# Performance work log

Measured on AMD Instinct MI355X. Metric: run time of the kernel, lower is better.

## Reference

```python
import jax, jax.numpy as jnp
import numpy as np

LOG_2PI = float(np.log(2.0 * np.pi))


def setup_inputs() -> dict:
    key = jax.random.key(0)
    k1, k2, k3 = jax.random.split(key, 3)
    B, T, F, K = 16, 1024, 1024, 500
    X = jax.random.normal(k1, (B, T, F), dtype=jnp.float32)
    mu = jax.random.normal(k2, (K, F), dtype=jnp.float32)
    # cov must be positive for log(cov); uniform in [0.5, 1.5)
    cov = jax.random.uniform(k3, (K, F), dtype=jnp.float32) + 0.5
    return {"X": X, "mu": mu, "cov": cov}


def reference(X, mu, cov):
    # Diagonal-covariance GMM log-likelihoods: out[b,t,k] = log N(X[b,t]; mu[k], diag(cov[k]))
    # Algebraic expansion of 0.5*sum((x-mu)^2/cov) into two GEMMs + bias, avoiding
    # the BxTxKxF broadcast intermediate. Same math as the torch module.
    D = mu.shape[-1]
    inv_cov = 1.0 / cov                                   # (K, F)
    C = -0.5 * D * LOG_2PI - 0.5 * jnp.sum(jnp.log(cov), axis=-1)  # (K,)
    quad = jnp.einsum('btf,kf->btk', X * X, inv_cov)      # sum x^2/cov
    cross = jnp.einsum('btf,kf->btk', X, mu * inv_cov)    # sum x*mu/cov
    const = jnp.sum(mu * mu * inv_cov, axis=-1)           # (K,) sum mu^2/cov
    ULL = 0.5 * (quad - 2.0 * cross + const[None, None, :])
    return C[None, None, :] - ULL                         # (B, T, K)
```

## Files before the change

kernel.cpp:

```cpp
#include <hip/hip_runtime.h>
#include <hip/hip_bf16.h>


typedef __attribute__((ext_vector_type(8))) __bf16 bf16x8;
typedef __attribute__((ext_vector_type(4))) float  f32x4;

#define LOG_2PI 1.837877066409345339082f

constexpr int M_TOT = 16384;
constexpr int F_DIM = 1024;
constexpr int K_GMM = 500;
constexpr int N_PAD = 512;

constexpr int BM  = 128;
constexpr int BN  = 128;
constexpr int BKF = 32;
constexpr int NIT = F_DIM / BKF;

__device__ __forceinline__ void gload_lds16(const void* g, void* l) {
    __builtin_amdgcn_global_load_lds(
        (const __attribute__((address_space(1))) unsigned*)g,
        (__attribute__((address_space(3))) unsigned*)l, 16, 0, 0);
}

__device__ __forceinline__ unsigned pack_sq_x(float x) {
    __hip_bfloat162 h = __float22bfloat162_rn(make_float2(x * x, x));
    union { __hip_bfloat162 h; unsigned u; } cv;
    cv.h = h;
    return cv.u;
}

__global__ __launch_bounds__(256) void prep_w_kernel(
    const float* __restrict__ mu, const float* __restrict__ cov,
    unsigned* __restrict__ Wimg, float* __restrict__ bias)
{
    const int k = blockIdx.x;
    const int t = threadIdx.x;
    const int r  = k & 127;
    const int tt = k >> 7;
    const int rsw = r & 7;
    float sl = 0.f, sq = 0.f;
    #pragma unroll
    for (int j = 0; j < 4; ++j) {
        const int f  = t + j * 256;
        const int it = f >> 5;
        const int cc = (f >> 2) & 7;
        const int q  = f & 3;
        const int dw = (tt * 32 + it) * 4096 + r * 32 + ((cc ^ rsw) << 2) + q;
        if (k < K_GMM) {
            const float c = cov[k * F_DIM + f];
            const float m = mu[k * F_DIM + f];
            const float ic = 1.0f / c;
            __hip_bfloat162 h = __float22bfloat162_rn(make_float2(-0.5f * ic, m * ic));
            union { __hip_bfloat162 h; unsigned u; } cv; cv.h = h;
            Wimg[dw] = cv.u;
            sl += logf(c);
            sq += m * m * ic;
        } else {
            Wimg[dw] = 0u;
        }
    }
    #pragma unroll
    for (int off = 32; off > 0; off >>= 1) {
        sl += __shfl_down(sl, off, 64);
        sq += __shfl_down(sq, off, 64);
    }
    __shared__ float red[8];
    if ((t & 63) == 0) { red[(t >> 6) * 2] = sl; red[(t >> 6) * 2 + 1] = sq; }
    __syncthreads();
    if (t == 0) {
        const float SL = red[0] + red[2] + red[4] + red[6];
        const float SQ = red[1] + red[3] + red[5] + red[7];
        bias[k] = (k < K_GMM)
                ? (-0.5f * (F_DIM * LOG_2PI) - 0.5f * SL - 0.5f * SQ) : 0.f;
    }
}

__global__ __launch_bounds__(256, 2) void gemm_kernel(
    const float* __restrict__ X, const unsigned* __restrict__ Wimg,
    const float* __restrict__ bias, float* __restrict__ out)
{
    __shared__ __align__(16) char smem[81920];
    float* ep = reinterpret_cast<float*>(smem);

    const int bid    = blockIdx.x;
    const int m_base = (bid & 127) * BM;
    const int n_tile = bid >> 7;
    const int n_base = n_tile * BN;

    const int tid  = threadIdx.x;
    const int lane = tid & 63;
    const int wv   = tid >> 6;
    const int wr   = (wv >> 1) * 64;
    const int wc   = (wv & 1) * 64;
    const int hi   = lane >> 4;
    const int lo   = lane & 15;
    const int lsw  = lo & 7;

    const int sr = tid >> 1;
    const int sh = tid & 1;

    const float4* Xv   = reinterpret_cast<const float4*>(X);
    const char*   Wimc = reinterpret_cast<const char*>(Wimg);

    f32x4 acc[4][4];
    #pragma unroll
    for (int a = 0; a < 4; ++a)
        #pragma unroll
        for (int b = 0; b < 4; ++b)
            acc[a][b] = (f32x4){0.f, 0.f, 0.f, 0.f};

    auto stageB = [&](int itS, int bufS) {
        const char* gs = Wimc + (size_t)(n_tile * 32 + itS) * 16384;
        #pragma unroll
        for (int i = 0; i < 4; ++i)
            gload_lds16(gs + i * 4096 + wv * 1024 + lane * 16,
                        smem + 32768 + bufS * 16384 + i * 4096 + wv * 1024);
    };
    auto loadA = [&](int itS, float4* ar) {
        #pragma unroll
        for (int j = 0; j < 4; ++j)
            ar[j] = Xv[(m_base + sr) * (F_DIM / 4) + itS * 8 + sh * 4 + j];
    };
    auto packA = [&](const float4* ar, int ab) {
        unsigned short* Ad = reinterpret_cast<unsigned short*>(smem + ab * 16384);
        #pragma unroll
        for (int j = 0; j < 4; ++j) {
            const int chunk = (sh * 4 + j) ^ (sr & 7);
            uint4 wa;
            wa.x = pack_sq_x(ar[j].x);
            wa.y = pack_sq_x(ar[j].y);
            wa.z = pack_sq_x(ar[j].z);
            wa.w = pack_sq_x(ar[j].w);
            *reinterpret_cast<uint4*>(&Ad[sr * 64 + chunk * 8]) = wa;
        }
    };
    auto compute = [&](int ab, int bb) {
        const unsigned short* Asc =
            reinterpret_cast<const unsigned short*>(smem + ab * 16384);
        const unsigned short* Bsc =
            reinterpret_cast<const unsigned short*>(smem + 32768 + bb * 16384);
        #pragma unroll
        for (int c = 0; c < 2; ++c) {
            bf16x8 af[4], bf[4];
            #pragma unroll
            for (int a = 0; a < 4; ++a) {
                const int row   = wr + a * 16 + lo;
                const int chunk = (c * 4 + hi) ^ lsw;
                af[a] = *reinterpret_cast<const bf16x8*>(&Asc[row * 64 + chunk * 8]);
            }
            #pragma unroll
            for (int b = 0; b < 4; ++b) {
                const int row   = wc + b * 16 + lo;
                const int chunk = (c * 4 + hi) ^ lsw;
                bf[b] = *reinterpret_cast<const bf16x8*>(&Bsc[row * 64 + chunk * 8]);
            }
            #pragma unroll
            for (int a = 0; a < 4; ++a)
                #pragma unroll
                for (int b = 0; b < 4; ++b)
                    acc[a][b] = __builtin_amdgcn_mfma_f32_16x16x32_bf16(
                        af[a], bf[b], acc[a][b], 0, 0, 0);
        }
    };

    float4 aA[4], aB[4];
    stageB(0, 0);
    loadA(0, aB);
    stageB(1, 1);
    loadA(1, aA);
    packA(aB, 0);
    asm volatile("s_waitcnt vmcnt(8) lgkmcnt(0)" ::: "memory");
    __builtin_amdgcn_s_barrier();
    __builtin_amdgcn_sched_barrier(0);

    for (int it = 0; it < NIT; it += 2) {
        const int b0 = it % 3;
        const int b1 = (it + 1) % 3;
        const int b2 = (it + 2) % 3;
        const int b3 = (it + 3) % 3;

        if (it + 2 < NIT) { stageB(it + 2, b2); loadA(it + 2, aB); }
        compute(0, b0);
        packA(aA, 1);
        if (it + 2 < NIT)
            asm volatile("s_waitcnt vmcnt(8) lgkmcnt(0)" ::: "memory");
        else
            asm volatile("s_waitcnt vmcnt(0) lgkmcnt(0)" ::: "memory");
        __builtin_amdgcn_s_barrier();
        __builtin_amdgcn_sched_barrier(0);

        if (it + 3 < NIT) { stageB(it + 3, b3); loadA(it + 3, aA); }
        compute(1, b1);
        if (it + 2 < NIT) packA(aB, 0);
        if (it + 3 < NIT)
            asm volatile("s_waitcnt vmcnt(8) lgkmcnt(0)" ::: "memory");
        else
            asm volatile("s_waitcnt vmcnt(0) lgkmcnt(0)" ::: "memory");
        __builtin_amdgcn_s_barrier();
        __builtin_amdgcn_sched_barrier(0);
    }

    const int ncols = (K_GMM - n_base < BN) ? (K_GMM - n_base) : BN;
    #pragma unroll
    for (int p = 0; p < 2; ++p) {
        if (p) __syncthreads();
        if ((wv >> 1) == p) {
            #pragma unroll
            for (int b = 0; b < 4; ++b) {
                const int col = wc + b * 16 + lo;
                const float bv = bias[n_base + col];
                #pragma unroll
                for (int a = 0; a < 4; ++a)
                    #pragma unroll
                    for (int i = 0; i < 4; ++i)
                        ep[(a * 16 + hi * 4 + i) * 128 + col] = acc[a][b][i] + bv;
            }
        }
        __syncthreads();
        #pragma unroll
        for (int k = 0; k < 8; ++k) {
            const int f    = k * 256 + tid;
            const int row  = f >> 5;
            const int slot = f & 31;
            if (slot * 4 < ncols) {
                const float4 v = *reinterpret_cast<const float4*>(&ep[row * 128 + slot * 4]);
                *reinterpret_cast<float4*>(
                    &out[(size_t)(m_base + p * 64 + row) * K_GMM + n_base + slot * 4]) = v;
            }
        }
    }
}

extern "C" void kernel_launch(void* const* d_in, const int* in_sizes, int n_in,
                              void* d_out, int out_size, void* d_ws, size_t ws_size,
                              hipStream_t stream)
{
    (void)in_sizes; (void)n_in; (void)out_size; (void)ws_size;
    const float* X   = (const float*)d_in[0];
    const float* mu  = (const float*)d_in[1];
    const float* cov = (const float*)d_in[2];
    float* out = (float*)d_out;

    unsigned* Wimg = (unsigned*)d_ws;
    float*    bias = (float*)((char*)d_ws + (size_t)N_PAD * F_DIM * 4);

    prep_w_kernel<<<dim3(N_PAD), dim3(256), 0, stream>>>(mu, cov, Wimg, bias);
    gemm_kernel<<<dim3((M_TOT / BM) * (N_PAD / BN)), dim3(256), 0, stream>>>(X, Wimg, bias, out);
}
```

Measured before the change: 54.60 us.

## Load X directly into MFMA fragments from global, bypassing LDS staging

Each wave now reads its X rows straight from global memory into registers and converts them to bf16 (x², x) fragments for the MFMAs, instead of packing into LDS and reading back. This removes LDS writes/reads for the A operand and shrinks shared memory to only the B triple buffer plus epilogue. In exchange, each X element is fetched by two waves, global loads are less contiguous, and register pressure grows with 16 float4 buffers.

```diff
diff --git a/kernel.cpp b/kernel.cpp
--- a/kernel.cpp
+++ b/kernel.cpp
@@ -28,6 +28,15 @@
     union { __hip_bfloat162 h; unsigned u; } cv;
     cv.h = h;
     return cv.u;
+}
+
+__device__ __forceinline__ bf16x8 pack_frag(float4 v) {
+    union { uint4 u; bf16x8 h; } r;
+    r.u.x = pack_sq_x(v.x);
+    r.u.y = pack_sq_x(v.y);
+    r.u.z = pack_sq_x(v.z);
+    r.u.w = pack_sq_x(v.w);
+    return r.h;
 }
 
 __global__ __launch_bounds__(256) void prep_w_kernel(
@@ -80,7 +89,7 @@
     const float* __restrict__ X, const unsigned* __restrict__ Wimg,
     const float* __restrict__ bias, float* __restrict__ out)
 {
-    __shared__ __align__(16) char smem[81920];
+    __shared__ __align__(16) char smem[49152];
     float* ep = reinterpret_cast<float*>(smem);
 
     const int bid    = blockIdx.x;
@@ -97,12 +106,14 @@
     const int lo   = lane & 15;
     const int lsw  = lo & 7;
 
-    const int sr = tid >> 1;
-    const int sh = tid & 1;
-
     const float4* Xv   = reinterpret_cast<const float4*>(X);
     const char*   Wimc = reinterpret_cast<const char*>(Wimg);
 
+    int arow[4];
+    #pragma unroll
+    for (int a = 0; a < 4; ++a)
+        arow[a] = (m_base + wr + a * 16 + lo) * (F_DIM / 4) + hi;
+
     f32x4 acc[4][4];
     #pragma unroll
     for (int a = 0; a < 4; ++a)
@@ -115,40 +126,21 @@
         #pragma unroll
         for (int i = 0; i < 4; ++i)
             gload_lds16(gs + i * 4096 + wv * 1024 + lane * 16,
-                        smem + 32768 + bufS * 16384 + i * 4096 + wv * 1024);
+                        smem + bufS * 16384 + i * 4096 + wv * 1024);
     };
     auto loadA = [&](int itS, float4* ar) {
         #pragma unroll
-        for (int j = 0; j < 4; ++j)
-            ar[j] = Xv[(m_base + sr) * (F_DIM / 4) + itS * 8 + sh * 4 + j];
+        for (int a = 0; a < 4; ++a)
+            #pragma unroll
+            for (int c = 0; c < 2; ++c)
+                ar[a * 2 + c] = Xv[arow[a] + itS * 8 + c * 4];
     };
-    auto packA = [&](const float4* ar, int ab) {
-        unsigned short* Ad = reinterpret_cast<unsigned short*>(smem + ab * 16384);
-        #pragma unroll
-        for (int j = 0; j < 4; ++j) {
-            const int chunk = (sh * 4 + j) ^ (sr & 7);
-            uint4 wa;
-            wa.x = pack_sq_x(ar[j].x);
-            wa.y = pack_sq_x(ar[j].y);
-            wa.z = pack_sq_x(ar[j].z);
-            wa.w = pack_sq_x(ar[j].w);
-            *reinterpret_cast<uint4*>(&Ad[sr * 64 + chunk * 8]) = wa;
-        }
-    };
-    auto compute = [&](int ab, int bb) {
-        const unsigned short* Asc =
-            reinterpret_cast<const unsigned short*>(smem + ab * 16384);
+    auto mfmas = [&](const bf16x8* pa, int bb) {
         const unsigned short* Bsc =
-            reinterpret_cast<const unsigned short*>(smem + 32768 + bb * 16384);
+            reinterpret_cast<const unsigned short*>(smem + bb * 16384);
         #pragma unroll
         for (int c = 0; c < 2; ++c) {
-            bf16x8 af[4], bf[4];
-            #pragma unroll
-            for (int a = 0; a < 4; ++a) {
-                const int row   = wr + a * 16 + lo;
-                const int chunk = (c * 4 + hi) ^ lsw;
-                af[a] = *reinterpret_cast<const bf16x8*>(&Asc[row * 64 + chunk * 8]);
-            }
+            bf16x8 bf[4];
             #pragma unroll
             for (int b = 0; b < 4; ++b) {
                 const int row   = wc + b * 16 + lo;
@@ -160,17 +152,16 @@
                 #pragma unroll
                 for (int b = 0; b < 4; ++b)
                     acc[a][b] = __builtin_amdgcn_mfma_f32_16x16x32_bf16(
-                        af[a], bf[b], acc[a][b], 0, 0, 0);
+                        pa[a * 2 + c], bf[b], acc[a][b], 0, 0, 0);
         }
     };
 
-    float4 aA[4], aB[4];
+    float4 aA[8], aB[8];
+    loadA(0, aA);
     stageB(0, 0);
-    loadA(0, aB);
     stageB(1, 1);
-    loadA(1, aA);
-    packA(aB, 0);
-    asm volatile("s_waitcnt vmcnt(8) lgkmcnt(0)" ::: "memory");
+    loadA(1, aB);
+    asm volatile("s_waitcnt vmcnt(12) lgkmcnt(0)" ::: "memory");
     __builtin_amdgcn_s_barrier();
     __builtin_amdgcn_sched_barrier(0);
 
@@ -180,25 +171,35 @@
         const int b2 = (it + 2) % 3;
         const int b3 = (it + 3) % 3;
 
-        if (it + 2 < NIT) { stageB(it + 2, b2); loadA(it + 2, aB); }
-        compute(0, b0);
-        packA(aA, 1);
-        if (it + 2 < NIT)
-            asm volatile("s_waitcnt vmcnt(8) lgkmcnt(0)" ::: "memory");
-        else
-            asm volatile("s_waitcnt vmcnt(0) lgkmcnt(0)" ::: "memory");
-        __builtin_amdgcn_s_barrier();
-        __builtin_amdgcn_sched_barrier(0);
-
-        if (it + 3 < NIT) { stageB(it + 3, b3); loadA(it + 3, aA); }
-        compute(1, b1);
-        if (it + 2 < NIT) packA(aB, 0);
-        if (it + 3 < NIT)
-            asm volatile("s_waitcnt vmcnt(8) lgkmcnt(0)" ::: "memory");
-        else
-            asm volatile("s_waitcnt vmcnt(0) lgkmcnt(0)" ::: "memory");
-        __builtin_amdgcn_s_barrier();
-        __builtin_amdgcn_sched_barrier(0);
+        {
+            if (it + 2 < NIT) stageB(it + 2, b2);
+            bf16x8 pa[8];
+            #pragma unroll
+            for (int k = 0; k < 8; ++k) pa[k] = pack_frag(aA[k]);
+            if (it + 2 < NIT) loadA(it + 2, aA);
+            mfmas(pa, b0);
+            if (it + 2 < NIT)
+                asm volatile("s_waitcnt vmcnt(12) lgkmcnt(0)" ::: "memory");
+            else
+                asm volatile("s_waitcnt vmcnt(0) lgkmcnt(0)" ::: "memory");
+            __builtin_amdgcn_s_barrier();
+            __builtin_amdgcn_sched_barrier(0);
+        }
+
+        {
+            if (it + 3 < NIT) stageB(it + 3, b3);
+            bf16x8 pb[8];
+            #pragma unroll
+            for (int k = 0; k < 8; ++k) pb[k] = pack_frag(aB[k]);
+            if (it + 3 < NIT) loadA(it + 3, aB);
+            mfmas(pb, b1);
+            if (it + 3 < NIT)
+                asm volatile("s_waitcnt vmcnt(12) lgkmcnt(0)" ::: "memory");
+            else
+                asm volatile("s_waitcnt vmcnt(0) lgkmcnt(0)" ::: "memory");
+            __builtin_amdgcn_s_barrier();
+            __builtin_amdgcn_sched_barrier(0);
+        }
     }
 
     const int ncols = (K_GMM - n_base < BN) ? (K_GMM - n_base) : BN;
```

New measurement: 84.84 us. 1.55x slower.

## Load B fragments directly from global into registers, drop LDS staging for W

Applied to the files above, without the earlier changes.

The weight image is re-laid out in the prep kernel so that each wave's MFMA B fragments are contiguous per lane. The GEMM then loads them straight into registers with double buffering instead of staging them through LDS with global_load_lds. This shrinks shared memory from 80KB to 32KB and removes the B LDS reads. The A pipeline is rescheduled with a deeper register prefetch, and s_setprio is added around the MFMAs. The cost is more VGPR pressure and global loads issued per wave rather than shared across the block.

```diff
diff --git a/kernel.cpp b/kernel.cpp
--- a/kernel.cpp
+++ b/kernel.cpp
@@ -16,12 +16,6 @@
 constexpr int BN  = 128;
 constexpr int BKF = 32;
 constexpr int NIT = F_DIM / BKF;
-
-__device__ __forceinline__ void gload_lds16(const void* g, void* l) {
-    __builtin_amdgcn_global_load_lds(
-        (const __attribute__((address_space(1))) unsigned*)g,
-        (__attribute__((address_space(3))) unsigned*)l, 16, 0, 0);
-}
 
 __device__ __forceinline__ unsigned pack_sq_x(float x) {
     __hip_bfloat162 h = __float22bfloat162_rn(make_float2(x * x, x));
@@ -36,26 +30,29 @@
 {
     const int k = blockIdx.x;
     const int t = threadIdx.x;
-    const int r  = k & 127;
-    const int tt = k >> 7;
-    const int rsw = r & 7;
+    const int tt  = k >> 7;
+    const int wch = (k >> 6) & 1;
+    const int b   = (k >> 4) & 3;
+    const int lo  = k & 15;
     float sl = 0.f, sq = 0.f;
     #pragma unroll
     for (int j = 0; j < 4; ++j) {
-        const int f  = t + j * 256;
-        const int it = f >> 5;
-        const int cc = (f >> 2) & 7;
-        const int q  = f & 3;
-        const int dw = (tt * 32 + it) * 4096 + r * 32 + ((cc ^ rsw) << 2) + q;
+        const int d  = t + j * 256;
+        const int it = d >> 5;
+        const int c  = (d >> 4) & 1;
+        const int hi = (d >> 2) & 3;
+        const int jj = d & 3;
+        const int dw = ((((tt * 2 + wch) * 32 + it) * 8) + (b * 2 + c)) * 256
+                     + (hi * 16 + lo) * 4 + jj;
         if (k < K_GMM) {
-            const float c = cov[k * F_DIM + f];
-            const float m = mu[k * F_DIM + f];
-            const float ic = 1.0f / c;
-            __hip_bfloat162 h = __float22bfloat162_rn(make_float2(-0.5f * ic, m * ic));
-            union { __hip_bfloat162 h; unsigned u; } cv; cv.h = h;
-            Wimg[dw] = cv.u;
-            sl += logf(c);
-            sq += m * m * ic;
+            const float cv_ = cov[k * F_DIM + d];
+            const float m_  = mu[k * F_DIM + d];
+            const float ic  = 1.0f / cv_;
+            __hip_bfloat162 h = __float22bfloat162_rn(make_float2(-0.5f * ic, m_ * ic));
+            union { __hip_bfloat162 h; unsigned u; } cvt; cvt.h = h;
+            Wimg[dw] = cvt.u;
+            sl += logf(cv_);
+            sq += m_ * m_ * ic;
         } else {
             Wimg[dw] = 0u;
         }
@@ -80,7 +77,7 @@
     const float* __restrict__ X, const unsigned* __restrict__ Wimg,
     const float* __restrict__ bias, float* __restrict__ out)
 {
-    __shared__ __align__(16) char smem[81920];
+    __shared__ __align__(16) char smem[32768];
     float* ep = reinterpret_cast<float*>(smem);
 
     const int bid    = blockIdx.x;
@@ -92,7 +89,8 @@
     const int lane = tid & 63;
     const int wv   = tid >> 6;
     const int wr   = (wv >> 1) * 64;
-    const int wc   = (wv & 1) * 64;
+    const int wch  = wv & 1;
+    const int wc   = wch * 64;
     const int hi   = lane >> 4;
     const int lo   = lane & 15;
     const int lsw  = lo & 7;
@@ -100,8 +98,9 @@
     const int sr = tid >> 1;
     const int sh = tid & 1;
 
-    const float4* Xv   = reinterpret_cast<const float4*>(X);
-    const char*   Wimc = reinterpret_cast<const char*>(Wimg);
+    const float4* Xv = reinterpret_cast<const float4*>(X);
+    const bf16x8* Wf = reinterpret_cast<const bf16x8*>(Wimg);
+    const int wbase = (n_tile * 2 + wch) * 32 * 8 * 64;
 
     f32x4 acc[4][4];
     #pragma unroll
@@ -110,13 +109,6 @@
         for (int b = 0; b < 4; ++b)
             acc[a][b] = (f32x4){0.f, 0.f, 0.f, 0.f};
 
-    auto stageB = [&](int itS, int bufS) {
-        const char* gs = Wimc + (size_t)(n_tile * 32 + itS) * 16384;
-        #pragma unroll
-        for (int i = 0; i < 4; ++i)
-            gload_lds16(gs + i * 4096 + wv * 1024 + lane * 16,
-                        smem + 32768 + bufS * 16384 + i * 4096 + wv * 1024);
-    };
     auto loadA = [&](int itS, float4* ar) {
         #pragma unroll
         for (int j = 0; j < 4; ++j)
@@ -135,14 +127,18 @@
             *reinterpret_cast<uint4*>(&Ad[sr * 64 + chunk * 8]) = wa;
         }
     };
-    auto compute = [&](int ab, int bb) {
+    auto loadB = [&](int itS, bf16x8* br) {
+        #pragma unroll
+        for (int f = 0; f < 8; ++f)
+            br[f] = Wf[wbase + (itS * 8 + f) * 64 + lane];
+    };
+    auto mfmas = [&](int ab, const bf16x8* br) {
         const unsigned short* Asc =
             reinterpret_cast<const unsigned short*>(smem + ab * 16384);
-        const unsigned short* Bsc =
-            reinterpret_cast<const unsigned short*>(smem + 32768 + bb * 16384);
+        bf16x8 af[4];
+        __builtin_amdgcn_s_setprio(1);
         #pragma unroll
         for (int c = 0; c < 2; ++c) {
-            bf16x8 af[4], bf[4];
             #pragma unroll
             for (int a = 0; a < 4; ++a) {
                 const int row   = wr + a * 16 + lo;
@@ -150,53 +146,41 @@
                 af[a] = *reinterpret_cast<const bf16x8*>(&Asc[row * 64 + chunk * 8]);
             }
             #pragma unroll
-            for (int b = 0; b < 4; ++b) {
-                const int row   = wc + b * 16 + lo;
-                const int chunk = (c * 4 + hi) ^ lsw;
-                bf[b] = *reinterpret_cast<const bf16x8*>(&Bsc[row * 64 + chunk * 8]);
-            }
-            #pragma unroll
             for (int a = 0; a < 4; ++a)
                 #pragma unroll
                 for (int b = 0; b < 4; ++b)
                     acc[a][b] = __builtin_amdgcn_mfma_f32_16x16x32_bf16(
-                        af[a], bf[b], acc[a][b], 0, 0, 0);
-        }
+                        af[a], br[b * 2 + c], acc[a][b], 0, 0, 0);
+        }
+        __builtin_amdgcn_s_setprio(0);
     };
 
     float4 aA[4], aB[4];
-    stageB(0, 0);
-    loadA(0, aB);
-    stageB(1, 1);
-    loadA(1, aA);
-    packA(aB, 0);
-    asm volatile("s_waitcnt vmcnt(8) lgkmcnt(0)" ::: "memory");
+    bf16x8 b0[8], b1[8];
+    loadA(0, aA);
+    loadB(0, b0);
+    loadA(1, aB);
+    loadB(1, b1);
+    packA(aA, 0);
+    loadA(2, aA);
+    asm volatile("s_waitcnt lgkmcnt(0)" ::: "memory");
     __builtin_amdgcn_s_barrier();
     __builtin_amdgcn_sched_barrier(0);
 
     for (int it = 0; it < NIT; it += 2) {
-        const int b0 = it % 3;
-        const int b1 = (it + 1) % 3;
-        const int b2 = (it + 2) % 3;
-        const int b3 = (it + 3) % 3;
-
-        if (it + 2 < NIT) { stageB(it + 2, b2); loadA(it + 2, aB); }
-        compute(0, b0);
-        packA(aA, 1);
-        if (it + 2 < NIT)
-            asm volatile("s_waitcnt vmcnt(8) lgkmcnt(0)" ::: "memory");
-        else
-            asm volatile("s_waitcnt vmcnt(0) lgkmcnt(0)" ::: "memory");
+        packA(aB, 1);
+        if (it + 3 < NIT) loadA(it + 3, aB);
+        mfmas(0, b0);
+        if (it + 2 < NIT) loadB(it + 2, b0);
+        asm volatile("s_waitcnt lgkmcnt(0)" ::: "memory");
         __builtin_amdgcn_s_barrier();
         __builtin_amdgcn_sched_barrier(0);
 
-        if (it + 3 < NIT) { stageB(it + 3, b3); loadA(it + 3, aA); }
-        compute(1, b1);
-        if (it + 2 < NIT) packA(aB, 0);
-        if (it + 3 < NIT)
-            asm volatile("s_waitcnt vmcnt(8) lgkmcnt(0)" ::: "memory");
-        else
-            asm volatile("s_waitcnt vmcnt(0) lgkmcnt(0)" ::: "memory");
+        if (it + 2 < NIT) packA(aA, 0);
+        if (it + 4 < NIT) loadA(it + 4, aA);
+        mfmas(1, b1);
+        if (it + 3 < NIT) loadB(it + 3, b1);
+        asm volatile("s_waitcnt lgkmcnt(0)" ::: "memory");
         __builtin_amdgcn_s_barrier();
         __builtin_amdgcn_sched_barrier(0);
     }
```

New measurement: 56.11 us. 2.8% more time.
